# Optimization experiments

Measured on AMD Instinct MI355X. Metric: run time of the kernel, lower is better.

The kernel has to match this reference:

```python
import jax, jax.numpy as jnp
import numpy as np

B, L, D, E = 32, 1024, 1024, 100  # batch, seq len, encoded_num, max_entities
Q_MAX = 200  # question tokens occupy [0, q_q_len); entities start after Q_MAX


def setup_inputs() -> dict:
    key = jax.random.key(0)
    k1, k2, k3, k4, k5, k6 = jax.random.split(key, 6)
    q_enc = jax.random.normal(k1, (B, L, D), dtype=jnp.float32)
    hint = jax.random.normal(k2, (B, L, 1), dtype=jnp.float32)
    q_q_len = jax.random.randint(k3, (B,), 150, Q_MAX + 1, dtype=jnp.int32)
    # entity ranges: entity e of batch b spans tokens (r0+1 .. r1-1), 3..7 tokens each,
    # laid out non-overlapping after the question region
    lens = np.asarray(jax.random.randint(k4, (B, E), 4, 9))  # r1 - r0
    starts = np.broadcast_to(Q_MAX + np.arange(E)[None, :] * 8, (B, E))
    entity_ranges = jnp.asarray(np.stack([starts, starts + lens], axis=-1), dtype=jnp.int32)
    W_attn = jax.random.normal(k5, (D + 1, D), dtype=jnp.float32) * 0.02  # nn.Linear(D, D+1)
    b_attn = jnp.zeros((D + 1,), jnp.float32)
    none_entity = jax.random.normal(k6, (1, D), dtype=jnp.float32) * 0.02
    return dict(q_enc=q_enc, hint=hint, W_attn=W_attn, b_attn=b_attn,
                none_entity=none_entity, q_q_len=q_q_len, entity_ranges=entity_ranges)


def reference(q_enc, hint, W_attn, b_attn, none_entity, q_q_len, entity_ranges):
    pos = jnp.arange(L)
    r0 = entity_ranges[..., 0]  # [B, E]
    r1 = entity_ranges[..., 1]
    # torch slice q_enc[b, r0+1:r1, :]  ->  mask pos in (r0, r1)
    ent_mask = ((pos[None, None, :] > r0[..., None]) &
                (pos[None, None, :] < r1[..., None])).astype(q_enc.dtype)  # [B, E, L]
    # ragged gather + segment-sum (zero-padding then sum == masked sum)
    encoded_entity = jnp.einsum('bel,bld->bed', ent_mask, q_enc)  # [B, E, D]
    encoded_entity = jnp.concatenate(
        [encoded_entity, jnp.broadcast_to(none_entity[None], (B, 1, D))], axis=1)  # [B, E+1, D]
    ent_proj = encoded_entity @ W_attn.T + b_attn  # [B, E+1, D+1]
    qv = jnp.concatenate([q_enc, hint], axis=-1)  # question_vectors with hint feature, [B, L, D+1]
    scores = jnp.einsum('blf,bef->ble', qv, ent_proj)  # [B, L, E+1]
    co_att = jax.nn.softmax(scores, axis=-1)
    # original only computes rows :q_q_len[b]; mask padded question rows to zero
    qmask = (pos[None, :] < q_q_len[:, None]).astype(co_att.dtype)[..., None]
    co_att = co_att * qmask
    att = jnp.minimum(jnp.sum(co_att, axis=1), 1.0)[:, :-1]  # clamp(max=1), drop none-entity col
    return att, co_att
```

## Files before the change

### kernel.cpp

```cpp
#include <hip/hip_runtime.h>
#include <hip/hip_bf16.h>

typedef unsigned short u16;
typedef __attribute__((ext_vector_type(8))) short short8;
typedef __attribute__((ext_vector_type(4))) float f32x4;

#define B_ 32
#define L_ 1024
#define D_ 1024
#define E_ 100
#define E1_ 101
#define M2_ (B_ * E1_)
#define M2P_ 3328
#define QBLK_ 16
#define NT3_ 13
#define ZROW0_ (NT3_ * QBLK_)

#define MFMA16(a, b, c) __builtin_amdgcn_mfma_f32_16x16x32_bf16((a), (b), (c), 0, 0, 0)

__device__ __forceinline__ void split2(float x, u16& h, u16& l) {
    __hip_bfloat16 bh = __float2bfloat16(x);
    float r = x - __bfloat162float(bh);
    __hip_bfloat16 bl = __float2bfloat16(r);
    h = __builtin_bit_cast(u16, bh);
    l = __builtin_bit_cast(u16, bl);
}

__device__ __forceinline__ void gload16(const void* g, void* l) {
    __builtin_amdgcn_global_load_lds(
        (const __attribute__((address_space(1))) unsigned int*)g,
        (__attribute__((address_space(3))) unsigned int*)l, 16, 0, 0);
}

__global__ __launch_bounds__(256) void k_zerofill(float* __restrict__ co_att) {
    int b = blockIdx.y;
    float4* base = (float4*)&co_att[((size_t)b * L_ + ZROW0_) * E1_];
    const int n4 = (L_ - ZROW0_) * E1_ / 4;
    float4 z = make_float4(0.f, 0.f, 0.f, 0.f);
    for (int i = blockIdx.x * 256 + threadIdx.x; i < n4; i += gridDim.x * 256)
        base[i] = z;
}

__global__ __launch_bounds__(256) void k_encode(const float* __restrict__ q_enc,
                                                const float* __restrict__ none_ent,
                                                const float* __restrict__ W,
                                                const float* __restrict__ bias,
                                                const int* __restrict__ ranges,
                                                u16* __restrict__ enc_hi, u16* __restrict__ enc_lo,
                                                float* __restrict__ ep_last) {
    __shared__ float red4[4];
    int be = blockIdx.x;
    int b = be / E1_, e = be - b * E1_;
    int t = threadIdx.x, c = t * 4;
    float4 acc;
    if (e == E_) {
        acc = *(const float4*)&none_ent[c];
    } else {
        acc = make_float4(0.f, 0.f, 0.f, 0.f);
        int r0 = ranges[(b * E_ + e) * 2 + 0];
        int r1 = ranges[(b * E_ + e) * 2 + 1];
        for (int l = r0 + 1; l < r1; ++l) {
            float4 v = *(const float4*)&q_enc[((size_t)b * L_ + l) * D_ + c];
            acc.x += v.x; acc.y += v.y; acc.z += v.z; acc.w += v.w;
        }
    }
    union { u16 u[4]; float2 f; } ph, pl;
    split2(acc.x, ph.u[0], pl.u[0]); split2(acc.y, ph.u[1], pl.u[1]);
    split2(acc.z, ph.u[2], pl.u[2]); split2(acc.w, ph.u[3], pl.u[3]);
    *(float2*)&enc_hi[(size_t)be * 1024 + c] = ph.f;
    *(float2*)&enc_lo[(size_t)be * 1024 + c] = pl.f;
    const float* w1k = W + (size_t)1024 * 1024;
    float4 wv = *(const float4*)&w1k[c];
    float s = acc.x * wv.x + acc.y * wv.y + acc.z * wv.z + acc.w * wv.w;
    #pragma unroll
    for (int off = 32; off; off >>= 1) s += __shfl_down(s, off);
    if ((t & 63) == 0) red4[t >> 6] = s;
    __syncthreads();
    if (t == 0) ep_last[be] = red4[0] + red4[1] + red4[2] + red4[3] + bias[1024];
}

__global__ __launch_bounds__(256) void k_wsplit(const float* __restrict__ W,
                                                u16* __restrict__ w_hi, u16* __restrict__ w_lo) {
    int r = blockIdx.x, c = threadIdx.x * 4;
    float4 v = *(const float4*)&W[(size_t)r * 1024 + c];
    union { u16 u[4]; float2 f; } ph, pl;
    split2(v.x, ph.u[0], pl.u[0]); split2(v.y, ph.u[1], pl.u[1]);
    split2(v.z, ph.u[2], pl.u[2]); split2(v.w, ph.u[3], pl.u[3]);
    *(float2*)&w_hi[(size_t)r * 1024 + c] = ph.f;
    *(float2*)&w_lo[(size_t)r * 1024 + c] = pl.f;
}

__global__ __launch_bounds__(256, 2) void k_entproj(const u16* __restrict__ A_hi, const u16* __restrict__ A_lo,
                                                    const u16* __restrict__ B_hi, const u16* __restrict__ B_lo,
                                                    const float* __restrict__ bias,
                                                    u16* __restrict__ ep_hi, u16* __restrict__ ep_lo) {
    __shared__ __attribute__((aligned(16))) u16 Ah[128 * 64], Al[128 * 64], Bh[64 * 64], Bl[64 * 64];
    int tid = threadIdx.x;
    int m0 = blockIdx.y * 128, n0 = blockIdx.x * 64;
    int w = tid >> 6, lane = tid & 63, lr = lane & 15, lg = lane >> 4;
    int wr = w >> 1, wc = w & 1;
    f32x4 zero = {0.f, 0.f, 0.f, 0.f};
    f32x4 acc[4][2];
    #pragma unroll
    for (int i = 0; i < 4; ++i) { acc[i][0] = zero; acc[i][1] = zero; }
    for (int k0 = 0; k0 < 1024; k0 += 64) {
        #pragma unroll
        for (int j = 0; j < 4; ++j) {
            int slot = w * 256 + j * 64 + lane;
            int r = slot >> 3, s = slot & 7;
            int g = (s ^ (r & 7)) << 3;
            size_t ga = (size_t)(m0 + r) * 1024 + k0 + g;
            int ld = (w * 256 + j * 64) * 8;
            gload16(&A_hi[ga], &Ah[ld]);
            gload16(&A_lo[ga], &Al[ld]);
        }
        #pragma unroll
        for (int j = 0; j < 2; ++j) {
            int slot = w * 128 + j * 64 + lane;
            int r = slot >> 3, s = slot & 7;
            int g = (s ^ (r & 7)) << 3;
            size_t gb = (size_t)(n0 + r) * 1024 + k0 + g;
            int ld = (w * 128 + j * 64) * 8;
            gload16(&B_hi[gb], &Bh[ld]);
            gload16(&B_lo[gb], &Bl[ld]);
        }
        __syncthreads();
        #pragma unroll
        for (int half = 0; half < 2; ++half) {
            int sk = half * 4 + lg;
            short8 a_h[4], a_l[4], b_h[2], b_l[2];
            #pragma unroll
            for (int mf = 0; mf < 4; ++mf) {
                int R = wr * 64 + mf * 16 + lr;
                int ad = R * 64 + ((sk ^ (R & 7)) << 3);
                a_h[mf] = __builtin_bit_cast(short8, *(const float4*)&Ah[ad]);
                a_l[mf] = __builtin_bit_cast(short8, *(const float4*)&Al[ad]);
            }
            #pragma unroll
            for (int nf = 0; nf < 2; ++nf) {
                int R = wc * 32 + nf * 16 + lr;
                int ad = R * 64 + ((sk ^ (R & 7)) << 3);
                b_h[nf] = __builtin_bit_cast(short8, *(const float4*)&Bh[ad]);
                b_l[nf] = __builtin_bit_cast(short8, *(const float4*)&Bl[ad]);
            }
            #pragma unroll
            for (int mf = 0; mf < 4; ++mf)
                #pragma unroll
                for (int nf = 0; nf < 2; ++nf) {
                    acc[mf][nf] = MFMA16(a_h[mf], b_h[nf], acc[mf][nf]);
                    acc[mf][nf] = MFMA16(a_h[mf], b_l[nf], acc[mf][nf]);
                    acc[mf][nf] = MFMA16(a_l[mf], b_h[nf], acc[mf][nf]);
                }
        }
        __syncthreads();
    }
    #pragma unroll
    for (int mf = 0; mf < 4; ++mf)
        #pragma unroll
        for (int nf = 0; nf < 2; ++nf)
            #pragma unroll
            for (int reg = 0; reg < 4; ++reg) {
                int m = m0 + wr * 64 + mf * 16 + lg * 4 + reg;
                if (m < M2_) {
                    int n = n0 + wc * 32 + nf * 16 + lr;
                    float v = acc[mf][nf][reg] + bias[n];
                    u16 h, l;
                    split2(v, h, l);
                    ep_hi[(size_t)m * 1024 + n] = h;
                    ep_lo[(size_t)m * 1024 + n] = l;
                }
            }
}

__global__ __launch_bounds__(256, 3) void k_scores(const float* __restrict__ q_enc,
                                                   const float* __restrict__ hint,
                                                   const u16* __restrict__ ep_hi, const u16* __restrict__ ep_lo,
                                                   const float* __restrict__ ep_last,
                                                   const int* __restrict__ qlen,
                                                   float* __restrict__ co_att,
                                                   float* __restrict__ partial) {
    __shared__ __attribute__((aligned(16))) u16 Ah[16 * 64], Al[16 * 64], Bh[128 * 64], Bl[128 * 64];
    __shared__ float Ss[16 * 113];
    __shared__ float red[QBLK_][16];
    int b = blockIdx.y, mt = blockIdx.x, l0 = mt * QBLK_;
    int tid = threadIdx.x;
    int qn = qlen[b];
    if (l0 >= qn) {
        float* base = &co_att[((size_t)b * L_ + l0) * E1_];
        float4 z = make_float4(0.f, 0.f, 0.f, 0.f);
        for (int i = tid; i < QBLK_ * E1_ / 4; i += 256)
            *(float4*)&base[i * 4] = z;
        for (int e = tid; e < E1_; e += 256)
            partial[((size_t)b * NT3_ + mt) * E1_ + e] = 0.f;
        return;
    }
    int w = tid >> 6, lane = tid & 63, lr = lane & 15, lg = lane >> 4;
    int nb = w * 2, nc = (w == 3) ? 1 : 2;
    int sb = w * 256;
    f32x4 zero = {0.f, 0.f, 0.f, 0.f};
    f32x4 acc[2] = {zero, zero};
    for (int k0 = 0; k0 < 1024; k0 += 64) {
        {
            #pragma unroll
            for (int j = 0; j < 4; ++j) {
                int slot = sb + j * 64 + lane;
                int r = slot >> 3, s = slot & 7;
                int g = (s ^ (r & 7)) << 3;
                size_t gb = ((size_t)b * E1_ + r) * 1024 + k0 + g;
                int ld = (sb + j * 64) * 8;
                gload16(&ep_hi[gb], &Bh[ld]);
                gload16(&ep_lo[gb], &Bl[ld]);
            }
        }
        if (tid < 128) {
            int r = tid >> 3, s = tid & 7;
            const float* src = &q_enc[((size_t)b * L_ + l0 + r) * D_ + k0 + s * 8];
            float4 x0 = *(const float4*)src, x1 = *(const float4*)(src + 4);
            float xs[8] = {x0.x, x0.y, x0.z, x0.w, x1.x, x1.y, x1.z, x1.w};
            short8 hv, lv;
            #pragma unroll
            for (int j = 0; j < 8; ++j) {
                u16 hh, ll;
                split2(xs[j], hh, ll);
                hv[j] = (short)hh; lv[j] = (short)ll;
            }
            int dst = r * 64 + ((s ^ (r & 7)) << 3);
            *(float4*)&Ah[dst] = __builtin_bit_cast(float4, hv);
            *(float4*)&Al[dst] = __builtin_bit_cast(float4, lv);
        }
        __syncthreads();
        #pragma unroll
        for (int ks = 0; ks < 2; ++ks) {
            int sk = ks * 4 + lg;
            int adA = lr * 64 + ((sk ^ (lr & 7)) << 3);
            short8 ah = __builtin_bit_cast(short8, *(const float4*)&Ah[adA]);
            short8 al = __builtin_bit_cast(short8, *(const float4*)&Al[adA]);
            #pragma unroll
            for (int nf = 0; nf < 2; ++nf) {
                if (nf < nc) {
                    int rB = (nb + nf) * 16 + lr;
                    int adB = rB * 64 + ((sk ^ (rB & 7)) << 3);
                    short8 bh = __builtin_bit_cast(short8, *(const float4*)&Bh[adB]);
                    short8 bl = __builtin_bit_cast(short8, *(const float4*)&Bl[adB]);
                    acc[nf] = MFMA16(ah, bh, acc[nf]);
                    acc[nf] = MFMA16(ah, bl, acc[nf]);
                    acc[nf] = MFMA16(al, bh, acc[nf]);
                }
            }
        }
        __syncthreads();
    }
    #pragma unroll
    for (int nf = 0; nf < 2; ++nf)
        if (nf < nc) {
            #pragma unroll
            for (int reg = 0; reg < 4; ++reg)
                Ss[(lg * 4 + reg) * 113 + (nb + nf) * 16 + lr] = acc[nf][reg];
        }
    __syncthreads();
    int l = tid & 15, eg = tid >> 4;
    float h = hint[(size_t)b * L_ + l0 + l];
    float sc[7];
    #pragma unroll
    for (int j = 0; j < 7; ++j) {
        int e = eg + 16 * j;
        sc[j] = (e < E1_) ? (Ss[l * 113 + e] + h * ep_last[b * E1_ + e]) : -3.4e38f;
    }
    float mloc = -3.4e38f;
    #pragma unroll
    for (int j = 0; j < 7; ++j) mloc = fmaxf(mloc, sc[j]);
    red[l][eg] = mloc;
    __syncthreads();
    float m = red[l][0];
    #pragma unroll
    for (int k = 1; k < 16; ++k) m = fmaxf(m, red[l][k]);
    __syncthreads();
    float p[7];
    float sloc = 0.f;
    #pragma unroll
    for (int j = 0; j < 7; ++j) {
        p[j] = 0.f;
        if (eg + 16 * j < E1_) { p[j] = __expf(sc[j] - m); sloc += p[j]; }
    }
    red[l][eg] = sloc;
    __syncthreads();
    float ssum = 0.f;
    #pragma unroll
    for (int k = 0; k < 16; ++k) ssum += red[l][k];
    float inv = 1.f / ssum;
    bool valid = (l0 + l) < qn;
    float maskv = valid ? inv : 0.f;
    float* row = &co_att[((size_t)b * L_ + l0 + l) * E1_];
    #pragma unroll
    for (int j = 0; j < 7; ++j) {
        int e = eg + 16 * j;
        if (e < E1_) row[e] = p[j] * maskv;
    }
    #pragma unroll
    for (int j = 0; j < 7; ++j) {
        int e = eg + 16 * j;
        float v = (e < E1_) ? p[j] * maskv : 0.f;
        v += __shfl_xor(v, 1);  v += __shfl_xor(v, 2);
        v += __shfl_xor(v, 4);  v += __shfl_xor(v, 8);
        if ((tid & 15) == 0 && e < E1_)
            partial[((size_t)b * NT3_ + mt) * E1_ + e] = v;
    }
}

__global__ __launch_bounds__(256) void k_final(const float* __restrict__ partial,
                                               float* __restrict__ att) {
    int i = blockIdx.x * 256 + threadIdx.x;
    if (i >= B_ * E_) return;
    int b = i / E_, e = i % E_;
    float s = 0.f;
    #pragma unroll
    for (int k = 0; k < NT3_; ++k) s += partial[((size_t)b * NT3_ + k) * E1_ + e];
    att[i] = fminf(s, 1.f);
}

extern "C" void kernel_launch(void* const* d_in, const int* in_sizes, int n_in,
                              void* d_out, int out_size, void* d_ws, size_t ws_size,
                              hipStream_t stream) {
    const float* q_enc    = (const float*)d_in[0];
    const float* hint     = (const float*)d_in[1];
    const float* W        = (const float*)d_in[2];
    const float* bias     = (const float*)d_in[3];
    const float* none_ent = (const float*)d_in[4];
    const int*   qlen     = (const int*)d_in[5];
    const int*   ranges   = (const int*)d_in[6];

    float* att    = (float*)d_out;
    float* co_att = att + (size_t)B_ * E_;

    u16* enc_hi = (u16*)d_ws;
    u16* enc_lo = enc_hi + (size_t)M2P_ * 1024;
    u16* w_hi   = enc_lo + (size_t)M2P_ * 1024;
    u16* w_lo   = w_hi + (size_t)1024 * 1024;
    u16* ep_hi  = w_lo + (size_t)1024 * 1024;
    u16* ep_lo  = ep_hi + (size_t)M2P_ * 1024;
    float* ep_last = (float*)(ep_lo + (size_t)M2P_ * 1024);
    float* part    = ep_last + M2P_;

    k_zerofill<<<dim3(20, B_), 256, 0, stream>>>(co_att);
    k_encode<<<M2_, 256, 0, stream>>>(q_enc, none_ent, W, bias, ranges, enc_hi, enc_lo, ep_last);
    k_wsplit<<<1024, 256, 0, stream>>>(W, w_hi, w_lo);
    k_entproj<<<dim3(16, 26), 256, 0, stream>>>(enc_hi, enc_lo, w_hi, w_lo, bias, ep_hi, ep_lo);
    k_scores<<<dim3(NT3_, B_), 256, 0, stream>>>(q_enc, hint, ep_hi, ep_lo, ep_last, qlen, co_att, part);
    k_final<<<13, 256, 0, stream>>>(part, att);
}
```

Measured before the change: 85.44 us.

## Merge prep kernels into one launch and halve entproj M-tile for more blocks

```diff
diff --git a/kernel.cpp b/kernel.cpp
--- a/kernel.cpp
+++ b/kernel.cpp
@@ -15,6 +15,8 @@
 #define QBLK_ 16
 #define NT3_ 13
 #define ZROW0_ (NT3_ * QBLK_)
+#define NZF_ 640
+#define NPREP_ (M2_ + 1024 + NZF_)
 
 #define MFMA16(a, b, c) __builtin_amdgcn_mfma_f32_16x16x32_bf16((a), (b), (c), 0, 0, 0)
 
@@ -32,95 +34,86 @@
         (__attribute__((address_space(3))) unsigned int*)l, 16, 0, 0);
 }
 
-__global__ __launch_bounds__(256) void k_zerofill(float* __restrict__ co_att) {
-    int b = blockIdx.y;
-    float4* base = (float4*)&co_att[((size_t)b * L_ + ZROW0_) * E1_];
-    const int n4 = (L_ - ZROW0_) * E1_ / 4;
-    float4 z = make_float4(0.f, 0.f, 0.f, 0.f);
-    for (int i = blockIdx.x * 256 + threadIdx.x; i < n4; i += gridDim.x * 256)
-        base[i] = z;
-}
-
-__global__ __launch_bounds__(256) void k_encode(const float* __restrict__ q_enc,
-                                                const float* __restrict__ none_ent,
-                                                const float* __restrict__ W,
-                                                const float* __restrict__ bias,
-                                                const int* __restrict__ ranges,
-                                                u16* __restrict__ enc_hi, u16* __restrict__ enc_lo,
-                                                float* __restrict__ ep_last) {
+__global__ __launch_bounds__(256) void k_prep(const float* __restrict__ q_enc,
+                                              const float* __restrict__ none_ent,
+                                              const float* __restrict__ W,
+                                              const float* __restrict__ bias,
+                                              const int* __restrict__ ranges,
+                                              u16* __restrict__ enc_hi, u16* __restrict__ enc_lo,
+                                              u16* __restrict__ w_hi, u16* __restrict__ w_lo,
+                                              float* __restrict__ ep_last,
+                                              float* __restrict__ co_att) {
     __shared__ float red4[4];
-    int be = blockIdx.x;
-    int b = be / E1_, e = be - b * E1_;
+    int u = blockIdx.x;
     int t = threadIdx.x, c = t * 4;
-    float4 acc;
-    if (e == E_) {
-        acc = *(const float4*)&none_ent[c];
+    if (u < M2_) {
+        int b = u / E1_, e = u - b * E1_;
+        float4 acc;
+        if (e == E_) {
+            acc = *(const float4*)&none_ent[c];
+        } else {
+            acc = make_float4(0.f, 0.f, 0.f, 0.f);
+            int r0 = ranges[(b * E_ + e) * 2 + 0];
+            int r1 = ranges[(b * E_ + e) * 2 + 1];
+            for (int l = r0 + 1; l < r1; ++l) {
+                float4 v = *(const float4*)&q_enc[((size_t)b * L_ + l) * D_ + c];
+                acc.x += v.x; acc.y += v.y; acc.z += v.z; acc.w += v.w;
+            }
+        }
+        union { u16 uu[4]; float2 f; } ph, pl;
+        split2(acc.x, ph.uu[0], pl.uu[0]); split2(acc.y, ph.uu[1], pl.uu[1]);
+        split2(acc.z, ph.uu[2], pl.uu[2]); split2(acc.w, ph.uu[3], pl.uu[3]);
+        *(float2*)&enc_hi[(size_t)u * 1024 + c] = ph.f;
+        *(float2*)&enc_lo[(size_t)u * 1024 + c] = pl.f;
+        const float* w1k = W + (size_t)1024 * 1024;
+        float4 wv = *(const float4*)&w1k[c];
+        float s = acc.x * wv.x + acc.y * wv.y + acc.z * wv.z + acc.w * wv.w;
+        #pragma unroll
+        for (int off = 32; off; off >>= 1) s += __shfl_down(s, off);
+        if ((t & 63) == 0) red4[t >> 6] = s;
+        __syncthreads();
+        if (t == 0) ep_last[u] = red4[0] + red4[1] + red4[2] + red4[3] + bias[1024];
+    } else if (u < M2_ + 1024) {
+        int r = u - M2_;
+        float4 v = *(const float4*)&W[(size_t)r * 1024 + c];
+        union { u16 uu[4]; float2 f; } ph, pl;
+        split2(v.x, ph.uu[0], pl.uu[0]); split2(v.y, ph.uu[1], pl.uu[1]);
+        split2(v.z, ph.uu[2], pl.uu[2]); split2(v.w, ph.uu[3], pl.uu[3]);
+        *(float2*)&w_hi[(size_t)r * 1024 + c] = ph.f;
+        *(float2*)&w_lo[(size_t)r * 1024 + c] = pl.f;
     } else {
-        acc = make_float4(0.f, 0.f, 0.f, 0.f);
-        int r0 = ranges[(b * E_ + e) * 2 + 0];
-        int r1 = ranges[(b * E_ + e) * 2 + 1];
-        for (int l = r0 + 1; l < r1; ++l) {
-            float4 v = *(const float4*)&q_enc[((size_t)b * L_ + l) * D_ + c];
-            acc.x += v.x; acc.y += v.y; acc.z += v.z; acc.w += v.w;
-        }
-    }
-    union { u16 u[4]; float2 f; } ph, pl;
-    split2(acc.x, ph.u[0], pl.u[0]); split2(acc.y, ph.u[1], pl.u[1]);
-    split2(acc.z, ph.u[2], pl.u[2]); split2(acc.w, ph.u[3], pl.u[3]);
-    *(float2*)&enc_hi[(size_t)be * 1024 + c] = ph.f;
-    *(float2*)&enc_lo[(size_t)be * 1024 + c] = pl.f;
-    const float* w1k = W + (size_t)1024 * 1024;
-    float4 wv = *(const float4*)&w1k[c];
-    float s = acc.x * wv.x + acc.y * wv.y + acc.z * wv.z + acc.w * wv.w;
-    #pragma unroll
-    for (int off = 32; off; off >>= 1) s += __shfl_down(s, off);
-    if ((t & 63) == 0) red4[t >> 6] = s;
-    __syncthreads();
-    if (t == 0) ep_last[be] = red4[0] + red4[1] + red4[2] + red4[3] + bias[1024];
-}
-
-__global__ __launch_bounds__(256) void k_wsplit(const float* __restrict__ W,
-                                                u16* __restrict__ w_hi, u16* __restrict__ w_lo) {
-    int r = blockIdx.x, c = threadIdx.x * 4;
-    float4 v = *(const float4*)&W[(size_t)r * 1024 + c];
-    union { u16 u[4]; float2 f; } ph, pl;
-    split2(v.x, ph.u[0], pl.u[0]); split2(v.y, ph.u[1], pl.u[1]);
-    split2(v.z, ph.u[2], pl.u[2]); split2(v.w, ph.u[3], pl.u[3]);
-    *(float2*)&w_hi[(size_t)r * 1024 + c] = ph.f;
-    *(float2*)&w_lo[(size_t)r * 1024 + c] = pl.f;
+        int zu = u - M2_ - 1024;
+        int b = zu / 20, part = zu % 20;
+        float4* base = (float4*)&co_att[((size_t)b * L_ + ZROW0_) * E1_];
+        const int n4 = (L_ - ZROW0_) * E1_ / 4;
+        float4 z = make_float4(0.f, 0.f, 0.f, 0.f);
+        for (int i = part * 256 + t; i < n4; i += 20 * 256)
+            base[i] = z;
+    }
 }
 
 __global__ __launch_bounds__(256, 2) void k_entproj(const u16* __restrict__ A_hi, const u16* __restrict__ A_lo,
                                                     const u16* __restrict__ B_hi, const u16* __restrict__ B_lo,
                                                     const float* __restrict__ bias,
                                                     u16* __restrict__ ep_hi, u16* __restrict__ ep_lo) {
-    __shared__ __attribute__((aligned(16))) u16 Ah[128 * 64], Al[128 * 64], Bh[64 * 64], Bl[64 * 64];
+    __shared__ __attribute__((aligned(16))) u16 Ah[64 * 64], Al[64 * 64], Bh[64 * 64], Bl[64 * 64];
     int tid = threadIdx.x;
-    int m0 = blockIdx.y * 128, n0 = blockIdx.x * 64;
+    int m0 = blockIdx.y * 64, n0 = blockIdx.x * 64;
     int w = tid >> 6, lane = tid & 63, lr = lane & 15, lg = lane >> 4;
     int wr = w >> 1, wc = w & 1;
     f32x4 zero = {0.f, 0.f, 0.f, 0.f};
-    f32x4 acc[4][2];
-    #pragma unroll
-    for (int i = 0; i < 4; ++i) { acc[i][0] = zero; acc[i][1] = zero; }
+    f32x4 acc[2][2] = {{zero, zero}, {zero, zero}};
     for (int k0 = 0; k0 < 1024; k0 += 64) {
-        #pragma unroll
-        for (int j = 0; j < 4; ++j) {
-            int slot = w * 256 + j * 64 + lane;
-            int r = slot >> 3, s = slot & 7;
-            int g = (s ^ (r & 7)) << 3;
-            size_t ga = (size_t)(m0 + r) * 1024 + k0 + g;
-            int ld = (w * 256 + j * 64) * 8;
-            gload16(&A_hi[ga], &Ah[ld]);
-            gload16(&A_lo[ga], &Al[ld]);
-        }
         #pragma unroll
         for (int j = 0; j < 2; ++j) {
             int slot = w * 128 + j * 64 + lane;
             int r = slot >> 3, s = slot & 7;
             int g = (s ^ (r & 7)) << 3;
+            size_t ga = (size_t)(m0 + r) * 1024 + k0 + g;
             size_t gb = (size_t)(n0 + r) * 1024 + k0 + g;
             int ld = (w * 128 + j * 64) * 8;
+            gload16(&A_hi[ga], &Ah[ld]);
+            gload16(&A_lo[ga], &Al[ld]);
             gload16(&B_hi[gb], &Bh[ld]);
             gload16(&B_lo[gb], &Bl[ld]);
         }
@@ -128,10 +121,10 @@
         #pragma unroll
         for (int half = 0; half < 2; ++half) {
             int sk = half * 4 + lg;
-            short8 a_h[4], a_l[4], b_h[2], b_l[2];
-            #pragma unroll
-            for (int mf = 0; mf < 4; ++mf) {
-                int R = wr * 64 + mf * 16 + lr;
+            short8 a_h[2], a_l[2], b_h[2], b_l[2];
+            #pragma unroll
+            for (int mf = 0; mf < 2; ++mf) {
+                int R = wr * 32 + mf * 16 + lr;
                 int ad = R * 64 + ((sk ^ (R & 7)) << 3);
                 a_h[mf] = __builtin_bit_cast(short8, *(const float4*)&Ah[ad]);
                 a_l[mf] = __builtin_bit_cast(short8, *(const float4*)&Al[ad]);
@@ -144,7 +137,7 @@
                 b_l[nf] = __builtin_bit_cast(short8, *(const float4*)&Bl[ad]);
             }
             #pragma unroll
-            for (int mf = 0; mf < 4; ++mf)
+            for (int mf = 0; mf < 2; ++mf)
                 #pragma unroll
                 for (int nf = 0; nf < 2; ++nf) {
                     acc[mf][nf] = MFMA16(a_h[mf], b_h[nf], acc[mf][nf]);
@@ -155,12 +148,12 @@
         __syncthreads();
     }
     #pragma unroll
-    for (int mf = 0; mf < 4; ++mf)
+    for (int mf = 0; mf < 2; ++mf)
         #pragma unroll
         for (int nf = 0; nf < 2; ++nf)
             #pragma unroll
             for (int reg = 0; reg < 4; ++reg) {
-                int m = m0 + wr * 64 + mf * 16 + lg * 4 + reg;
+                int m = m0 + wr * 32 + mf * 16 + lg * 4 + reg;
                 if (m < M2_) {
                     int n = n0 + wc * 32 + nf * 16 + lr;
                     float v = acc[mf][nf][reg] + bias[n];
@@ -341,10 +334,9 @@
     float* ep_last = (float*)(ep_lo + (size_t)M2P_ * 1024);
     float* part    = ep_last + M2P_;
 
-    k_zerofill<<<dim3(20, B_), 256, 0, stream>>>(co_att);
-    k_encode<<<M2_, 256, 0, stream>>>(q_enc, none_ent, W, bias, ranges, enc_hi, enc_lo, ep_last);
-    k_wsplit<<<1024, 256, 0, stream>>>(W, w_hi, w_lo);
-    k_entproj<<<dim3(16, 26), 256, 0, stream>>>(enc_hi, enc_lo, w_hi, w_lo, bias, ep_hi, ep_lo);
+    k_prep<<<NPREP_, 256, 0, stream>>>(q_enc, none_ent, W, bias, ranges,
+                                       enc_hi, enc_lo, w_hi, w_lo, ep_last, co_att);
+    k_entproj<<<dim3(16, 52), 256, 0, stream>>>(enc_hi, enc_lo, w_hi, w_lo, bias, ep_hi, ep_lo);
     k_scores<<<dim3(NT3_, B_), 256, 0, stream>>>(q_enc, hint, ep_hi, ep_lo, ep_last, qlen, co_att, part);
     k_final<<<13, 256, 0, stream>>>(part, att);
 }
```

Result: faster. 80.35 us (-6.0%).
